# Kernel tuning notes

Measured on AMD Instinct MI355X. Metric: run time of the kernel, lower is better.

The kernel has to match this reference:

```python
import jax, jax.numpy as jnp
import numpy as np

B, S, D_H, D_L, K, K_H, W = 4, 4096, 1024, 256, 64, 4, 9


def setup_inputs() -> dict:
    key = jax.random.key(0)
    ks = jax.random.split(key, 6)
    return {
        "inputs": jax.random.normal(ks[0], (B, S, D_H), jnp.float32),
        "W1": jax.random.normal(ks[1], (D_H, D_L), jnp.float32) * 0.02,
        "b1": jnp.zeros((D_L,), jnp.float32),
        "RME": jax.random.normal(ks[2], (D_L, K), jnp.float32),
        "K2": jax.random.normal(ks[3], (K_H, D_L, D_L), jnp.float32) * 0.02,
        "b2": jnp.zeros((D_L,), jnp.float32),
        "Wu": jax.random.normal(ks[4], (D_L, D_H), jnp.float32) * 0.02,
        "bu": jnp.zeros((D_H,), jnp.float32),
        "gamma": jnp.ones((D_H,), jnp.float32),
        "beta": jnp.zeros((D_H,), jnp.float32),
    }


def _memory_reorg(act, RMVs, k_h):
    # act: [B,S,d_l], RMVs: [B,S,k]
    R = jnp.transpose(RMVs, (0, 2, 1))  # [B,k,S]
    h_vars = jnp.mean((R - jnp.mean(R, axis=-1, keepdims=True)) ** 2, axis=-1)  # [B,k]
    top = jnp.argsort(-h_vars, axis=-1)[:, :k_h]                   # [B,k_h]
    h_max = jnp.take_along_axis(R, top[:, :, None], axis=1)        # [B,k_h,S]
    perm = jnp.argsort(h_max, axis=-1)                             # [B,k_h,S] permutation indices
    g = jnp.take_along_axis(act[:, None], perm[..., None], axis=2) # [B,k_h,S,d_l]
    return jnp.transpose(g, (0, 2, 1, 3))                          # [B,S,k_h,d_l]


def reference(inputs, W1, b1, RME, K2, b2, Wu, bu, gamma, beta):
    # DOWN_PROJECTION_1
    q = jax.nn.relu(jnp.einsum('bsh,hd->bsd', inputs, W1) + b1)    # [B,S,d_l]
    # RANDOM_PROJECTION
    RMVs = jnp.einsum('bsd,dk->bsk', q, RME)                       # [B,S,k]
    # Memory reorganization (variance-based argsort permutations)
    qp = _memory_reorg(q, RMVs, K_H)                               # [B,S,k_h,d_l]
    # DOWN_PROJECTION_2
    q2 = jax.nn.relu(jnp.einsum('bskd,kde->bse', qp, K2) + b2)     # [B,S,d_l]
    # Sliding-window key construction (edge windows replicated)
    half = (W - 1) // 2
    widx = jnp.arange(S - W + 1)[:, None] + jnp.arange(W)[None, :]  # [S-W+1, W]
    win = q2[:, widx]                                               # [B,S-W+1,W,d_l]
    first = jnp.broadcast_to(q2[:, None, :W], (B, half, W, D_L))
    last = jnp.broadcast_to(q2[:, None, S - W:], (B, half, W, D_L))
    keyt = jnp.concatenate([first, win, last], axis=1)              # [B,S,W,d_l]
    # Windowed attention
    f = jnp.sqrt(jnp.float32(D_L))
    scores = jax.nn.softmax(jnp.einsum('bsd,bswd->bsw', q2, keyt) / f, axis=-1)  # [B,S,W]
    # UP_PROJECTION on keys -> values
    val = jax.nn.relu(jnp.einsum('bswd,dh->bswh', keyt, Wu) + bu)   # [B,S,W,d_h]
    out = jnp.einsum('bswh,bsw->bsh', val, scores)                  # [B,S,d_h]
    # LayerNorm (keras default epsilon=1e-3) on residual
    x = out + inputs
    mu = jnp.mean(x, axis=-1, keepdims=True)
    var = jnp.mean((x - mu) ** 2, axis=-1, keepdims=True)
    return gamma * (x - mu) * jax.lax.rsqrt(var + 1e-3) + beta
```

## Files before the change

kernel.cpp:

```cpp
#include <hip/hip_runtime.h>

#define B_  4
#define S_  4096
#define DH  1024
#define DL  256
#define KK  64
#define KH  4
#define WW  9

typedef unsigned short ushort_t;
typedef _Float16 f16;
typedef _Float16 f16x8 __attribute__((ext_vector_type(8)));
typedef float  f32x4  __attribute__((ext_vector_type(4)));

__device__ __forceinline__ void gld_lds16(const void* g, void* lds_uniform_base) {
    __builtin_amdgcn_global_load_lds(
        (const __attribute__((address_space(1))) unsigned int*)g,
        (__attribute__((address_space(3))) unsigned int*)lds_uniform_base,
        16, 0, 0);
}

template<bool AFP32, bool GATHER, int OUTMODE>
__global__ __launch_bounds__(256)
void mfma_gemm_sm(const float* __restrict__ Af,
                  const ushort_t* __restrict__ Ah, const ushort_t* __restrict__ Al,
                  const ushort_t* __restrict__ Bh, const ushort_t* __restrict__ Bl,
                  const float* __restrict__ bias, float* __restrict__ C,
                  ushort_t* __restrict__ Ch, ushort_t* __restrict__ Cl,
                  const int* __restrict__ gidx, int K, int N, int nbx)
{
    __shared__ __align__(16) ushort_t Abuf[2][64 * 64 * 2];
    __shared__ __align__(16) ushort_t Bbuf[2][2][64 * 64];

    const int tid = threadIdx.x;
    const int w = tid >> 6, l = tid & 63;
    const int wm = w >> 1, wn = w & 1;
    const int lr = l & 15, lk = l >> 4;
    const int cpx = gridDim.x >> 3;
    const int orig = (blockIdx.x & 7) * cpx + (blockIdx.x >> 3);
    const int m0 = (orig / nbx) * 64, n0 = (orig % nbx) * 64;

    int rg[2][KH];
    if (GATHER) {
        const int r0 = tid >> 3;
        #pragma unroll
        for (int it = 0; it < 2; ++it)
            #pragma unroll
            for (int h = 0; h < KH; ++h)
                rg[it][h] = gidx[(m0 + it * 32 + r0) * KH + h];
    }

    auto stage = [&](int buf, int k0) {
        if (AFP32) {
            float* Asf = (float*)Abuf[buf];
            #pragma unroll
            for (int it = 0; it < 4; ++it) {
                const int c = it * 256 + tid;
                const int r = c >> 4, cc = c & 15;
                const int cs = cc ^ ((r & 7) << 1);
                gld_lds16(Af + (size_t)(m0 + r) * K + k0 + cs * 4, &Asf[(size_t)c * 4]);
            }
        } else {
            ushort_t* Ash = Abuf[buf];
            ushort_t* Asl = Abuf[buf] + 64 * 64;
            #pragma unroll
            for (int it = 0; it < 2; ++it) {
                const int c = it * 256 + tid;
                const int r = c >> 3, kp = c & 7;
                const int kl = kp ^ (r & 7);
                size_t offA;
                if (GATHER) {
                    offA = (size_t)rg[it][k0 >> 8] * DL + (k0 & (DL - 1)) + kl * 8;
                } else {
                    offA = (size_t)(m0 + r) * K + k0 + kl * 8;
                }
                gld_lds16(Ah + offA, &Ash[(size_t)c * 8]);
                gld_lds16(Al + offA, &Asl[(size_t)c * 8]);
            }
        }
        #pragma unroll
        for (int it = 0; it < 2; ++it) {
            const int c = it * 256 + tid;
            const int r = c >> 3, kp = c & 7;
            const int kl = kp ^ (r & 7);
            const size_t off = (size_t)(n0 + r) * K + k0 + kl * 8;
            gld_lds16(Bh + off, &Bbuf[buf][0][(size_t)c * 8]);
            gld_lds16(Bl + off, &Bbuf[buf][1][(size_t)c * 8]);
        }
    };

    f32x4 acc0[2][2] = {};
    f32x4 acc1[2][2] = {};

    stage(0, 0);
    __syncthreads();
    int cur = 0;
    for (int k0 = 0; k0 < K; k0 += 64) {
        if (k0 + 64 < K) stage(cur ^ 1, k0 + 64);

        #pragma unroll
        for (int ks = 0; ks < 2; ++ks) {
            f16x8 ah[2], al[2];
            #pragma unroll
            for (int mf = 0; mf < 2; ++mf) {
                const int row = wm * 32 + mf * 16 + lr;
                const int kb  = ks * 4 + lk;
                if (AFP32) {
                    const float* Asf = (const float*)Abuf[cur];
                    const int fo = row * 64 + ((kb ^ (row & 7)) << 3);
                    const f32x4 lo = *(const f32x4*)&Asf[fo];
                    const f32x4 hi = *(const f32x4*)&Asf[fo + 4];
                    const float xs[8] = {lo[0], lo[1], lo[2], lo[3],
                                         hi[0], hi[1], hi[2], hi[3]};
                    #pragma unroll
                    for (int e = 0; e < 8; ++e) {
                        const f16 h = (f16)xs[e];
                        const f16 lv = (f16)((xs[e] - (float)h) * 2048.0f);
                        ah[mf][e] = h;
                        al[mf][e] = lv;
                    }
                } else {
                    const ushort_t* Ash = Abuf[cur];
                    const ushort_t* Asl = Abuf[cur] + 64 * 64;
                    const int o = row * 64 + ((kb ^ (row & 7)) << 3);
                    ah[mf] = *(const f16x8*)&Ash[o];
                    al[mf] = *(const f16x8*)&Asl[o];
                }
            }
            #pragma unroll
            for (int nf = 0; nf < 2; ++nf) {
                const int row = wn * 32 + nf * 16 + lr;
                const int kb  = ks * 4 + lk;
                const int o   = row * 64 + ((kb ^ (row & 7)) << 3);
                const f16x8 bh = *(const f16x8*)&Bbuf[cur][0][o];
                const f16x8 bl = *(const f16x8*)&Bbuf[cur][1][o];
                #pragma unroll
                for (int mf = 0; mf < 2; ++mf) {
                    acc0[mf][nf] = __builtin_amdgcn_mfma_f32_16x16x32_f16(
                        ah[mf], bh, acc0[mf][nf], 0, 0, 0);
                    acc1[mf][nf] = __builtin_amdgcn_mfma_f32_16x16x32_f16(
                        ah[mf], bl, acc1[mf][nf], 0, 0, 0);
                    acc1[mf][nf] = __builtin_amdgcn_mfma_f32_16x16x32_f16(
                        al[mf], bh, acc1[mf][nf], 0, 0, 0);
                }
            }
        }
        __syncthreads();
        cur ^= 1;
    }

    float bv[2];
    #pragma unroll
    for (int nf = 0; nf < 2; ++nf)
        bv[nf] = bias[n0 + wn * 32 + nf * 16 + lr];
    #pragma unroll
    for (int mf = 0; mf < 2; ++mf)
        #pragma unroll
        for (int nf = 0; nf < 2; ++nf)
            #pragma unroll
            for (int r = 0; r < 4; ++r) {
                const int m = m0 + wm * 32 + mf * 16 + lk * 4 + r;
                const int n = n0 + wn * 32 + nf * 16 + lr;
                float x = acc0[mf][nf][r] + acc1[mf][nf][r] * (1.0f / 2048.0f) + bv[nf];
                x = fmaxf(x, 0.f);
                const f16 h = (f16)x;
                if (OUTMODE == 2) {
                    Ch[(size_t)m * N + n] = __builtin_bit_cast(ushort_t, h);
                } else {
                    C[(size_t)m * N + n] = x;
                    Ch[(size_t)m * N + n] = __builtin_bit_cast(ushort_t, h);
                    const f16 lo = (f16)((x - (float)h) * 2048.0f);
                    Cl[(size_t)m * N + n] = __builtin_bit_cast(ushort_t, lo);
                }
            }
}

__global__ __launch_bounds__(512)
void mfma_gemm1l(const ushort_t* __restrict__ Ah, const ushort_t* __restrict__ Bh,
                 const float* __restrict__ bias, ushort_t* __restrict__ Ch,
                 int K, int N, int nbx)
{
    __shared__ __align__(16) ushort_t Ash[2][128 * 64];
    __shared__ __align__(16) ushort_t Bsh[2][128 * 64];

    const int tid = threadIdx.x;
    const int w = tid >> 6, l = tid & 63;
    const int wm = w >> 1, wn = w & 1;
    const int lr = l & 15, lk = l >> 4;
    const int cpx = gridDim.x >> 3;
    const int orig = (blockIdx.x & 7) * cpx + (blockIdx.x >> 3);
    const int m0 = (orig / nbx) * 128, n0 = (orig % nbx) * 128;

    auto stage = [&](int buf, int k0) {
        #pragma unroll
        for (int it = 0; it < 2; ++it) {
            const int c = it * 512 + tid;
            const int r = c >> 3, kp = c & 7;
            const int kl = kp ^ (r & 7);
            const size_t offA = (size_t)(m0 + r) * K + k0 + kl * 8;
            const size_t offB = (size_t)(n0 + r) * K + k0 + kl * 8;
            gld_lds16(Ah + offA, &Ash[buf][(size_t)c * 8]);
            gld_lds16(Bh + offB, &Bsh[buf][(size_t)c * 8]);
        }
    };

    f32x4 acc0[2][4] = {};

    stage(0, 0);
    __syncthreads();
    int cur = 0;
    for (int k0 = 0; k0 < K; k0 += 64) {
        if (k0 + 64 < K) stage(cur ^ 1, k0 + 64);

        #pragma unroll
        for (int ks = 0; ks < 2; ++ks) {
            f16x8 ah[2];
            #pragma unroll
            for (int mf = 0; mf < 2; ++mf) {
                const int row = wm * 32 + mf * 16 + lr;
                const int kb  = ks * 4 + lk;
                ah[mf] = *(const f16x8*)&Ash[cur][row * 64 + ((kb ^ (row & 7)) << 3)];
            }
            #pragma unroll
            for (int nf = 0; nf < 4; ++nf) {
                const int row = wn * 64 + nf * 16 + lr;
                const int kb  = ks * 4 + lk;
                const f16x8 bh = *(const f16x8*)&Bsh[cur][row * 64 + ((kb ^ (row & 7)) << 3)];
                #pragma unroll
                for (int mf = 0; mf < 2; ++mf)
                    acc0[mf][nf] = __builtin_amdgcn_mfma_f32_16x16x32_f16(
                        ah[mf], bh, acc0[mf][nf], 0, 0, 0);
            }
        }
        __syncthreads();
        cur ^= 1;
    }

    float bv[4];
    #pragma unroll
    for (int nf = 0; nf < 4; ++nf)
        bv[nf] = bias[n0 + wn * 64 + nf * 16 + lr];
    #pragma unroll
    for (int mf = 0; mf < 2; ++mf)
        #pragma unroll
        for (int nf = 0; nf < 4; ++nf)
            #pragma unroll
            for (int r = 0; r < 4; ++r) {
                const int m = m0 + wm * 32 + mf * 16 + lk * 4 + r;
                const int n = n0 + wn * 64 + nf * 16 + lr;
                float x = acc0[mf][nf][r] + bv[nf];
                x = fmaxf(x, 0.f);
                const f16 hcv = (f16)x;
                Ch[(size_t)m * N + n] = __builtin_bit_cast(ushort_t, hcv);
            }
}

__global__ __launch_bounds__(256)
void tsplit2_kernel(const float* __restrict__ in, ushort_t* __restrict__ t0,
                    ushort_t* __restrict__ t1, int K, int N)
{
    __shared__ float tile[32][33];
    const int t = threadIdx.x;
    const int bk = blockIdx.x * 32, bn = blockIdx.y * 32;
    const int c = t & 31, rb = t >> 5;
    #pragma unroll
    for (int i = 0; i < 4; ++i) {
        const int r = rb + i * 8;
        tile[r][c] = in[(size_t)(bk + r) * N + bn + c];
    }
    __syncthreads();
    #pragma unroll
    for (int i = 0; i < 4; ++i) {
        const int rr = rb + i * 8;
        const float x = tile[c][rr];
        const f16 hv = (f16)x;
        const f16 lv = (f16)((x - (float)hv) * 2048.0f);
        const size_t o = (size_t)(bn + rr) * K + bk + c;
        t0[o] = __builtin_bit_cast(ushort_t, hv);
        t1[o] = __builtin_bit_cast(ushort_t, lv);
    }
}

__global__ __launch_bounds__(256)
void gemm_trans_kernel(const float* __restrict__ A, const float* __restrict__ Bm,
                       float* __restrict__ C, int M, int KA, int N)
{
    constexpr int BK = 16;
    __shared__ float Asb[BK][64 + 4];
    __shared__ float Bsb[BK][64 + 4];
    const int tid = threadIdx.x;
    const int tx = tid & 15, ty = tid >> 4;
    const int m0 = blockIdx.y * 64, n0 = blockIdx.x * 64;

    float acc[4][4] = {};
    const int lr = tid >> 2, lc = (tid & 3) << 2;
    const int kr = tid >> 4, nc = (tid & 15) << 2;

    for (int k0 = 0; k0 < KA; k0 += BK) {
        const float4 a4 = *reinterpret_cast<const float4*>(A + (size_t)(m0 + lr) * KA + k0 + lc);
        const float4 b4 = *reinterpret_cast<const float4*>(Bm + (size_t)(k0 + kr) * N + n0 + nc);
        Asb[lc + 0][lr] = a4.x; Asb[lc + 1][lr] = a4.y;
        Asb[lc + 2][lr] = a4.z; Asb[lc + 3][lr] = a4.w;
        *reinterpret_cast<float4*>(&Bsb[kr][nc]) = b4;
        __syncthreads();
        #pragma unroll
        for (int kk = 0; kk < BK; ++kk) {
            const float4 av = *reinterpret_cast<const float4*>(&Asb[kk][ty << 2]);
            const float4 bv = *reinterpret_cast<const float4*>(&Bsb[kk][tx << 2]);
            const float a[4] = {av.x, av.y, av.z, av.w};
            const float b[4] = {bv.x, bv.y, bv.z, bv.w};
            #pragma unroll
            for (int i = 0; i < 4; ++i)
                #pragma unroll
                for (int j = 0; j < 4; ++j)
                    acc[i][j] = fmaf(a[i], b[j], acc[i][j]);
        }
        __syncthreads();
    }
    #pragma unroll
    for (int i = 0; i < 4; ++i) {
        const int m = m0 + (ty << 2) + i;
        const int b = m >> 12, s = m & (S_ - 1);
        #pragma unroll
        for (int j = 0; j < 4; ++j) {
            const int n = n0 + (tx << 2) + j;
            C[(size_t)(b * N + n) * S_ + s] = acc[i][j];
        }
    }
}

__global__ __launch_bounds__(256)
void var_kernel(const float* __restrict__ rmvT, float* __restrict__ hvars)
{
    const int bk = blockIdx.x;
    const float* src = rmvT + (size_t)bk * S_;
    float s1 = 0.f, s2 = 0.f;
    for (int t = threadIdx.x; t < S_; t += 256) {
        const float v = src[t];
        s1 += v; s2 += v * v;
    }
    #pragma unroll
    for (int off = 32; off; off >>= 1) {
        s1 += __shfl_xor(s1, off);
        s2 += __shfl_xor(s2, off);
    }
    __shared__ float r1[4], r2[4];
    const int wave = threadIdx.x >> 6, lane = threadIdx.x & 63;
    if (lane == 0) { r1[wave] = s1; r2[wave] = s2; }
    __syncthreads();
    if (threadIdx.x == 0) {
        const float t1 = r1[0] + r1[1] + r1[2] + r1[3];
        const float t2 = r2[0] + r2[1] + r2[2] + r2[3];
        const float mu = t1 / (float)S_;
        hvars[bk] = t2 / (float)S_ - mu * mu;
    }
}

__global__ void topk_kernel(const float* __restrict__ hvars, int* __restrict__ topidx)
{
    const int b = threadIdx.x;
    if (b >= B_) return;
    float v[KK];
    for (int k = 0; k < KK; ++k) v[k] = hvars[b * KK + k];
    for (int i = 0; i < KH; ++i) {
        int best = 0; float bv = -3.4e38f;
        for (int k = 0; k < KK; ++k)
            if (v[k] > bv) { bv = v[k]; best = k; }
        topidx[b * KH + i] = best;
        v[best] = -3.4e38f;
    }
}

__global__ __launch_bounds__(256)
void rank_kernel(const float* __restrict__ rmvT, const int* __restrict__ topidx,
                 int* __restrict__ gidx)
{
    const int bi = blockIdx.x;
    const int b = bi >> 2, ih = bi & 3;
    const int k = topidx[b * KH + ih];
    const float* src = rmvT + (size_t)(b * KK + k) * S_;
    __shared__ __align__(16) unsigned long long keys[S_];
    __shared__ int partial[4][64];
    for (int t = threadIdx.x; t < S_; t += 256) {
        const unsigned bits = __builtin_bit_cast(unsigned, src[t]);
        const unsigned u = (bits & 0x80000000u) ? ~bits : (bits | 0x80000000u);
        keys[t] = ((unsigned long long)u << 12) | (unsigned)t;
    }
    __syncthreads();

    const int il = threadIdx.x & 63;
    const int chunk = threadIdx.x >> 6;
    const int i = blockIdx.y * 64 + il;
    const unsigned long long ki = keys[i];

    int cnt = 0;
    const int jbase = chunk << 10;
    #pragma unroll 8
    for (int jj = 0; jj < 1024; jj += 2) {
        const ulonglong2 k2 = *reinterpret_cast<const ulonglong2*>(&keys[jbase + jj]);
        cnt += (int)(k2.x < ki);
        cnt += (int)(k2.y < ki);
    }
    partial[chunk][il] = cnt;
    __syncthreads();
    if (threadIdx.x < 64) {
        const int rank = partial[0][threadIdx.x] + partial[1][threadIdx.x]
                       + partial[2][threadIdx.x] + partial[3][threadIdx.x];
        const int ii = blockIdx.y * 64 + threadIdx.x;
        gidx[((b << 12) + rank) * KH + ih] = (b << 12) + ii;
    }
}

__global__ __launch_bounds__(256)
void final_kernel(const ushort_t* __restrict__ vh, const ushort_t* __restrict__ q2h,
                  const float* __restrict__ inputs, const float* __restrict__ gamma,
                  const float* __restrict__ beta, float* __restrict__ out)
{
    const int bid = blockIdx.x;
    const int m0 = (((bid & 7) << 9) | (bid >> 3)) << 2;
    const int wave = threadIdx.x >> 6, lane = threadIdx.x & 63;
    const int m = m0 + wave;
    const int s = m & (S_ - 1), b = m >> 12;
    const int jb = (s < 4) ? 0 : (s >= S_ - 4 ? S_ - WW : s - 4);

    const ushort_t* vb = vh + (size_t)(b * S_ + jb) * DH;
    const float* inp = inputs + (size_t)m * DH;
    f16x8 varr[2][WW];
    float4 iv[2][2];
    #pragma unroll
    for (int c = 0; c < 2; ++c) {
        const int h = (c << 9) + (lane << 3);
        #pragma unroll
        for (int w = 0; w < WW; ++w)
            varr[c][w] = *reinterpret_cast<const f16x8*>(vb + (size_t)w * DH + h);
        iv[c][0] = *reinterpret_cast<const float4*>(inp + h);
        iv[c][1] = *reinterpret_cast<const float4*>(inp + h + 4);
    }

    const ushort4 qv4 = *reinterpret_cast<const ushort4*>(q2h + (size_t)m * DL + (lane << 2));
    const float qx = (float)__builtin_bit_cast(f16, qv4.x);
    const float qy = (float)__builtin_bit_cast(f16, qv4.y);
    const float qz = (float)__builtin_bit_cast(f16, qv4.z);
    const float qw = (float)__builtin_bit_cast(f16, qv4.w);
    const ushort_t* kbase = q2h + (size_t)(b * S_ + jb) * DL;
    float sc[WW];
    #pragma unroll
    for (int w = 0; w < WW; ++w) {
        const ushort4 kv4 = *reinterpret_cast<const ushort4*>(kbase + w * DL + (lane << 2));
        float d = qx * (float)__builtin_bit_cast(f16, kv4.x)
                + qy * (float)__builtin_bit_cast(f16, kv4.y)
                + qz * (float)__builtin_bit_cast(f16, kv4.z)
                + qw * (float)__builtin_bit_cast(f16, kv4.w);
        #pragma unroll
        for (int off = 32; off; off >>= 1) d += __shfl_xor(d, off);
        sc[w] = d * 0.0625f;
    }
    float mx = sc[0];
    #pragma unroll
    for (int w = 1; w < WW; ++w) mx = fmaxf(mx, sc[w]);
    float wgt[WW]; float sum = 0.f;
    #pragma unroll
    for (int w = 0; w < WW; ++w) { wgt[w] = __expf(sc[w] - mx); sum += wgt[w]; }
    const float inv = 1.f / sum;
    #pragma unroll
    for (int w = 0; w < WW; ++w) wgt[w] *= inv;

    float x[2][8];
    float s1 = 0.f, s2 = 0.f;
    #pragma unroll
    for (int c = 0; c < 2; ++c) {
        float acc[8] = {};
        #pragma unroll
        for (int w = 0; w < WW; ++w) {
            const f16x8 vv = varr[c][w];
            #pragma unroll
            for (int e = 0; e < 8; ++e)
                acc[e] = fmaf(wgt[w], (float)vv[e], acc[e]);
        }
        #pragma unroll
        for (int e = 0; e < 8; ++e) {
            const float ivv = (e < 4) ? (&iv[c][0].x)[e] : (&iv[c][1].x)[e - 4];
            acc[e] += ivv;
            x[c][e] = acc[e];
            s1 += acc[e];
            s2 += acc[e] * acc[e];
        }
    }

    #pragma unroll
    for (int off = 32; off; off >>= 1) {
        s1 += __shfl_xor(s1, off);
        s2 += __shfl_xor(s2, off);
    }
    const float mu = s1 / (float)DH;
    const float rs = rsqrtf(s2 / (float)DH - mu * mu + 0.001f);

    #pragma unroll
    for (int c = 0; c < 2; ++c) {
        const int h = (c << 9) + (lane << 3);
        #pragma unroll
        for (int half = 0; half < 2; ++half) {
            const float4 g  = *reinterpret_cast<const float4*>(gamma + h + half * 4);
            const float4 bt = *reinterpret_cast<const float4*>(beta + h + half * 4);
            float4 o;
            o.x = g.x * (x[c][half * 4 + 0] - mu) * rs + bt.x;
            o.y = g.y * (x[c][half * 4 + 1] - mu) * rs + bt.y;
            o.z = g.z * (x[c][half * 4 + 2] - mu) * rs + bt.z;
            o.w = g.w * (x[c][half * 4 + 3] - mu) * rs + bt.w;
            *reinterpret_cast<float4*>(out + (size_t)m * DH + h + half * 4) = o;
        }
    }
}

extern "C" void kernel_launch(void* const* d_in, const int* in_sizes, int n_in,
                              void* d_out, int out_size, void* d_ws, size_t ws_size,
                              hipStream_t stream)
{
    (void)in_sizes; (void)n_in; (void)out_size; (void)ws_size;
    const float* inputs = (const float*)d_in[0];
    const float* W1     = (const float*)d_in[1];
    const float* b1     = (const float*)d_in[2];
    const float* RME    = (const float*)d_in[3];
    const float* K2     = (const float*)d_in[4];
    const float* b2     = (const float*)d_in[5];
    const float* Wu     = (const float*)d_in[6];
    const float* bu     = (const float*)d_in[7];
    const float* gamma  = (const float*)d_in[8];
    const float* beta   = (const float*)d_in[9];
    float* out = (float*)d_out;

    char* ws = (char*)d_ws;
    const size_t MB = 1u << 20;
    ushort_t* vh  = (ushort_t*)(ws + 0 * MB);
    float*    q   = (float*)   (ws + 64 * MB);
    ushort_t* qh  = (ushort_t*)(ws + 80 * MB);
    ushort_t* ql  = (ushort_t*)(ws + 88 * MB);
    ushort_t* q2h = (ushort_t*)(ws + 112 * MB);
    float*    rmvT= (float*)   (ws + 128 * MB);
    float*    hvars  = (float*)(ws + 132 * MB);
    int*      topidx = (int*)  (ws + 132 * MB + 4096);
    int*      gidx   = (int*)  (ws + 132 * MB + 8192);
    ushort_t* w1th = (ushort_t*)(ws + 133 * MB);
    ushort_t* w1tl = w1th + (DH * DL);
    ushort_t* k2th = w1tl + (DH * DL);
    ushort_t* k2tl = k2th + (KH * DL * DL);
    ushort_t* wuth = k2tl + (KH * DL * DL);
    ushort_t* wutl = wuth + (DL * DH);

    const int M = B_ * S_;

    tsplit2_kernel<<<dim3(DH / 32, DL / 32), dim3(256), 0, stream>>>(W1, w1th, w1tl, DH, DL);
    tsplit2_kernel<<<dim3(KH * DL / 32, DL / 32), dim3(256), 0, stream>>>((const float*)K2, k2th, k2tl, KH * DL, DL);
    tsplit2_kernel<<<dim3(DL / 32, DH / 32), dim3(256), 0, stream>>>(Wu, wuth, wutl, DL, DH);

    mfma_gemm_sm<true, false, 1><<<dim3((DL / 64) * (M / 64)), dim3(256), 0, stream>>>(
        inputs, nullptr, nullptr, w1th, w1tl, b1, q, qh, ql, nullptr, DH, DL, DL / 64);
    gemm_trans_kernel<<<dim3(KK / 64, M / 64), dim3(256), 0, stream>>>(q, RME, rmvT, M, DL, KK);
    var_kernel<<<dim3(B_ * KK), dim3(256), 0, stream>>>(rmvT, hvars);
    topk_kernel<<<dim3(1), dim3(64), 0, stream>>>(hvars, topidx);
    rank_kernel<<<dim3(B_ * KH, S_ / 64), dim3(256), 0, stream>>>(rmvT, topidx, gidx);
    mfma_gemm_sm<false, true, 2><<<dim3((DL / 64) * (M / 64)), dim3(256), 0, stream>>>(
        nullptr, qh, ql, k2th, k2tl, b2, nullptr, q2h, nullptr, gidx, KH * DL, DL, DL / 64);
    mfma_gemm1l<<<dim3((DH / 128) * (M / 128)), dim3(512), 0, stream>>>(
        q2h, wuth, bu, vh, DL, DH, DH / 128);
    final_kernel<<<dim3(M / 4), dim3(256), 0, stream>>>(vh, q2h, inputs, gamma, beta, out);
}
```

Baseline: 195.6 us.

## Load A operands directly into registers and drop double-buffering in up-projection GEMM

```diff
diff --git a/kernel.cpp b/kernel.cpp
--- a/kernel.cpp
+++ b/kernel.cpp
@@ -20,16 +20,16 @@
         16, 0, 0);
 }
 
-template<bool AFP32, bool GATHER, int OUTMODE>
+template<bool AFP32, bool GATHER, int OUTMODE, int KT>
 __global__ __launch_bounds__(256)
-void mfma_gemm_sm(const float* __restrict__ Af,
+void gemm_adirect(const float* __restrict__ Af,
                   const ushort_t* __restrict__ Ah, const ushort_t* __restrict__ Al,
                   const ushort_t* __restrict__ Bh, const ushort_t* __restrict__ Bl,
                   const float* __restrict__ bias, float* __restrict__ C,
                   ushort_t* __restrict__ Ch, ushort_t* __restrict__ Cl,
-                  const int* __restrict__ gidx, int K, int N, int nbx)
-{
-    __shared__ __align__(16) ushort_t Abuf[2][64 * 64 * 2];
+                  const int* __restrict__ gidx, int N, int nbx)
+{
+    constexpr int NT = KT / 64;
     __shared__ __align__(16) ushort_t Bbuf[2][2][64 * 64];
 
     const int tid = threadIdx.x;
@@ -39,92 +39,66 @@
     const int cpx = gridDim.x >> 3;
     const int orig = (blockIdx.x & 7) * cpx + (blockIdx.x >> 3);
     const int m0 = (orig / nbx) * 64, n0 = (orig % nbx) * 64;
-
-    int rg[2][KH];
-    if (GATHER) {
-        const int r0 = tid >> 3;
-        #pragma unroll
-        for (int it = 0; it < 2; ++it)
-            #pragma unroll
-            for (int h = 0; h < KH; ++h)
-                rg[it][h] = gidx[(m0 + it * 32 + r0) * KH + h];
-    }
-
-    auto stage = [&](int buf, int k0) {
-        if (AFP32) {
-            float* Asf = (float*)Abuf[buf];
-            #pragma unroll
-            for (int it = 0; it < 4; ++it) {
-                const int c = it * 256 + tid;
-                const int r = c >> 4, cc = c & 15;
-                const int cs = cc ^ ((r & 7) << 1);
-                gld_lds16(Af + (size_t)(m0 + r) * K + k0 + cs * 4, &Asf[(size_t)c * 4]);
-            }
-        } else {
-            ushort_t* Ash = Abuf[buf];
-            ushort_t* Asl = Abuf[buf] + 64 * 64;
-            #pragma unroll
-            for (int it = 0; it < 2; ++it) {
-                const int c = it * 256 + tid;
-                const int r = c >> 3, kp = c & 7;
-                const int kl = kp ^ (r & 7);
-                size_t offA;
-                if (GATHER) {
-                    offA = (size_t)rg[it][k0 >> 8] * DL + (k0 & (DL - 1)) + kl * 8;
-                } else {
-                    offA = (size_t)(m0 + r) * K + k0 + kl * 8;
-                }
-                gld_lds16(Ah + offA, &Ash[(size_t)c * 8]);
-                gld_lds16(Al + offA, &Asl[(size_t)c * 8]);
-            }
-        }
+    const int ar0 = m0 + wm * 32 + lr;
+
+    f32x4 af0[2][2][2], af1[2][2][2];
+    f16x8 ahr0[2][2], alr0[2][2], ahr1[2][2], alr1[2][2];
+
+    auto stageB = [&](int buf, int k0) {
         #pragma unroll
         for (int it = 0; it < 2; ++it) {
             const int c = it * 256 + tid;
             const int r = c >> 3, kp = c & 7;
             const int kl = kp ^ (r & 7);
-            const size_t off = (size_t)(n0 + r) * K + k0 + kl * 8;
+            const size_t off = (size_t)(n0 + r) * KT + k0 + kl * 8;
             gld_lds16(Bh + off, &Bbuf[buf][0][(size_t)c * 8]);
             gld_lds16(Bl + off, &Bbuf[buf][1][(size_t)c * 8]);
         }
     };
+    auto loadAf = [&](f32x4 ar[2][2][2], int k0) {
+        #pragma unroll
+        for (int mf = 0; mf < 2; ++mf)
+            #pragma unroll
+            for (int ks = 0; ks < 2; ++ks) {
+                const float* p = Af + (size_t)(ar0 + mf * 16) * KT + k0 + ks * 32 + lk * 8;
+                ar[mf][ks][0] = *(const f32x4*)p;
+                ar[mf][ks][1] = *(const f32x4*)(p + 4);
+            }
+    };
+    auto loadAg = [&](f16x8 ha[2][2], f16x8 la[2][2], int k0) {
+        const int head = k0 >> 8, kk = k0 & (DL - 1);
+        #pragma unroll
+        for (int mf = 0; mf < 2; ++mf) {
+            const int row = gidx[(ar0 + mf * 16) * KH + head];
+            #pragma unroll
+            for (int ks = 0; ks < 2; ++ks) {
+                const size_t off = (size_t)row * DL + kk + ks * 32 + lk * 8;
+                ha[mf][ks] = *(const f16x8*)(Ah + off);
+                la[mf][ks] = *(const f16x8*)(Al + off);
+            }
+        }
+    };
 
     f32x4 acc0[2][2] = {};
     f32x4 acc1[2][2] = {};
 
-    stage(0, 0);
-    __syncthreads();
-    int cur = 0;
-    for (int k0 = 0; k0 < K; k0 += 64) {
-        if (k0 + 64 < K) stage(cur ^ 1, k0 + 64);
-
+    auto computeT = [&](f32x4 arf[2][2][2], f16x8 arh[2][2], f16x8 arl[2][2], int buf) {
         #pragma unroll
         for (int ks = 0; ks < 2; ++ks) {
             f16x8 ah[2], al[2];
             #pragma unroll
             for (int mf = 0; mf < 2; ++mf) {
-                const int row = wm * 32 + mf * 16 + lr;
-                const int kb  = ks * 4 + lk;
                 if (AFP32) {
-                    const float* Asf = (const float*)Abuf[cur];
-                    const int fo = row * 64 + ((kb ^ (row & 7)) << 3);
-                    const f32x4 lo = *(const f32x4*)&Asf[fo];
-                    const f32x4 hi = *(const f32x4*)&Asf[fo + 4];
-                    const float xs[8] = {lo[0], lo[1], lo[2], lo[3],
-                                         hi[0], hi[1], hi[2], hi[3]};
                     #pragma unroll
                     for (int e = 0; e < 8; ++e) {
-                        const f16 h = (f16)xs[e];
-                        const f16 lv = (f16)((xs[e] - (float)h) * 2048.0f);
+                        const float xv = (e < 4) ? arf[mf][ks][0][e] : arf[mf][ks][1][e - 4];
+                        const f16 h = (f16)xv;
                         ah[mf][e] = h;
-                        al[mf][e] = lv;
+                        al[mf][e] = (f16)((xv - (float)h) * 2048.0f);
                     }
                 } else {
-                    const ushort_t* Ash = Abuf[cur];
-                    const ushort_t* Asl = Abuf[cur] + 64 * 64;
-                    const int o = row * 64 + ((kb ^ (row & 7)) << 3);
-                    ah[mf] = *(const f16x8*)&Ash[o];
-                    al[mf] = *(const f16x8*)&Asl[o];
+                    ah[mf] = arh[mf][ks];
+                    al[mf] = arl[mf][ks];
                 }
             }
             #pragma unroll
@@ -132,8 +106,8 @@
                 const int row = wn * 32 + nf * 16 + lr;
                 const int kb  = ks * 4 + lk;
                 const int o   = row * 64 + ((kb ^ (row & 7)) << 3);
-                const f16x8 bh = *(const f16x8*)&Bbuf[cur][0][o];
-                const f16x8 bl = *(const f16x8*)&Bbuf[cur][1][o];
+                const f16x8 bh = *(const f16x8*)&Bbuf[buf][0][o];
+                const f16x8 bl = *(const f16x8*)&Bbuf[buf][1][o];
                 #pragma unroll
                 for (int mf = 0; mf < 2; ++mf) {
                     acc0[mf][nf] = __builtin_amdgcn_mfma_f32_16x16x32_f16(
@@ -145,8 +119,36 @@
                 }
             }
         }
-        __syncthreads();
-        cur ^= 1;
+    };
+
+    stageB(0, 0);
+    if (AFP32) loadAf(af0, 0); else loadAg(ahr0, alr0, 0);
+    asm volatile("s_waitcnt vmcnt(0)" ::: "memory");
+    __builtin_amdgcn_s_barrier();
+    __builtin_amdgcn_sched_barrier(0);
+
+    #pragma unroll 1
+    for (int t = 0; t < NT; t += 2) {
+        if (t + 1 < NT) {
+            stageB(1, (t + 1) * 64);
+            if (AFP32) loadAf(af1, (t + 1) * 64); else loadAg(ahr1, alr1, (t + 1) * 64);
+        }
+        computeT(af0, ahr0, alr0, 0);
+        if (t + 1 < NT) { asm volatile("s_waitcnt vmcnt(8)" ::: "memory"); }
+        else            { asm volatile("s_waitcnt vmcnt(0)" ::: "memory"); }
+        __builtin_amdgcn_s_barrier();
+        __builtin_amdgcn_sched_barrier(0);
+        if (t + 1 < NT) {
+            if (t + 2 < NT) {
+                stageB(0, (t + 2) * 64);
+                if (AFP32) loadAf(af0, (t + 2) * 64); else loadAg(ahr0, alr0, (t + 2) * 64);
+            }
+            computeT(af1, ahr1, alr1, 1);
+            if (t + 2 < NT) { asm volatile("s_waitcnt vmcnt(8)" ::: "memory"); }
+            else            { asm volatile("s_waitcnt vmcnt(0)" ::: "memory"); }
+            __builtin_amdgcn_s_barrier();
+            __builtin_amdgcn_sched_barrier(0);
+        }
     }
 
     float bv[2];
@@ -180,8 +182,8 @@
                  const float* __restrict__ bias, ushort_t* __restrict__ Ch,
                  int K, int N, int nbx)
 {
-    __shared__ __align__(16) ushort_t Ash[2][128 * 64];
-    __shared__ __align__(16) ushort_t Bsh[2][128 * 64];
+    __shared__ __align__(16) ushort_t Ash[128 * 64];
+    __shared__ __align__(16) ushort_t Bsh[128 * 64];
 
     const int tid = threadIdx.x;
     const int w = tid >> 6, l = tid & 63;
@@ -191,7 +193,9 @@
     const int orig = (blockIdx.x & 7) * cpx + (blockIdx.x >> 3);
     const int m0 = (orig / nbx) * 128, n0 = (orig % nbx) * 128;
 
-    auto stage = [&](int buf, int k0) {
+    f32x4 acc0[2][4] = {};
+
+    for (int k0 = 0; k0 < K; k0 += 64) {
         #pragma unroll
         for (int it = 0; it < 2; ++it) {
             const int c = it * 512 + tid;
@@ -199,18 +203,10 @@
             const int kl = kp ^ (r & 7);
             const size_t offA = (size_t)(m0 + r) * K + k0 + kl * 8;
             const size_t offB = (size_t)(n0 + r) * K + k0 + kl * 8;
-            gld_lds16(Ah + offA, &Ash[buf][(size_t)c * 8]);
-            gld_lds16(Bh + offB, &Bsh[buf][(size_t)c * 8]);
-        }
-    };
-
-    f32x4 acc0[2][4] = {};
-
-    stage(0, 0);
-    __syncthreads();
-    int cur = 0;
-    for (int k0 = 0; k0 < K; k0 += 64) {
-        if (k0 + 64 < K) stage(cur ^ 1, k0 + 64);
+            gld_lds16(Ah + offA, &Ash[(size_t)c * 8]);
+            gld_lds16(Bh + offB, &Bsh[(size_t)c * 8]);
+        }
+        __syncthreads();
 
         #pragma unroll
         for (int ks = 0; ks < 2; ++ks) {
@@ -219,13 +215,13 @@
             for (int mf = 0; mf < 2; ++mf) {
                 const int row = wm * 32 + mf * 16 + lr;
                 const int kb  = ks * 4 + lk;
-                ah[mf] = *(const f16x8*)&Ash[cur][row * 64 + ((kb ^ (row & 7)) << 3)];
+                ah[mf] = *(const f16x8*)&Ash[row * 64 + ((kb ^ (row & 7)) << 3)];
             }
             #pragma unroll
             for (int nf = 0; nf < 4; ++nf) {
                 const int row = wn * 64 + nf * 16 + lr;
                 const int kb  = ks * 4 + lk;
-                const f16x8 bh = *(const f16x8*)&Bsh[cur][row * 64 + ((kb ^ (row & 7)) << 3)];
+                const f16x8 bh = *(const f16x8*)&Bsh[row * 64 + ((kb ^ (row & 7)) << 3)];
                 #pragma unroll
                 for (int mf = 0; mf < 2; ++mf)
                     acc0[mf][nf] = __builtin_amdgcn_mfma_f32_16x16x32_f16(
@@ -233,7 +229,6 @@
             }
         }
         __syncthreads();
-        cur ^= 1;
     }
 
     float bv[4];
@@ -553,14 +548,14 @@
     tsplit2_kernel<<<dim3(KH * DL / 32, DL / 32), dim3(256), 0, stream>>>((const float*)K2, k2th, k2tl, KH * DL, DL);
     tsplit2_kernel<<<dim3(DL / 32, DH / 32), dim3(256), 0, stream>>>(Wu, wuth, wutl, DL, DH);
 
-    mfma_gemm_sm<true, false, 1><<<dim3((DL / 64) * (M / 64)), dim3(256), 0, stream>>>(
-        inputs, nullptr, nullptr, w1th, w1tl, b1, q, qh, ql, nullptr, DH, DL, DL / 64);
+    gemm_adirect<true, false, 1, DH><<<dim3((DL / 64) * (M / 64)), dim3(256), 0, stream>>>(
+        inputs, nullptr, nullptr, w1th, w1tl, b1, q, qh, ql, nullptr, DL, DL / 64);
     gemm_trans_kernel<<<dim3(KK / 64, M / 64), dim3(256), 0, stream>>>(q, RME, rmvT, M, DL, KK);
     var_kernel<<<dim3(B_ * KK), dim3(256), 0, stream>>>(rmvT, hvars);
     topk_kernel<<<dim3(1), dim3(64), 0, stream>>>(hvars, topidx);
     rank_kernel<<<dim3(B_ * KH, S_ / 64), dim3(256), 0, stream>>>(rmvT, topidx, gidx);
-    mfma_gemm_sm<false, true, 2><<<dim3((DL / 64) * (M / 64)), dim3(256), 0, stream>>>(
-        nullptr, qh, ql, k2th, k2tl, b2, nullptr, q2h, nullptr, gidx, KH * DL, DL, DL / 64);
+    gemm_adirect<false, true, 2, KH * DL><<<dim3((DL / 64) * (M / 64)), dim3(256), 0, stream>>>(
+        nullptr, qh, ql, k2th, k2tl, b2, nullptr, q2h, nullptr, gidx, DL, DL / 64);
     mfma_gemm1l<<<dim3((DH / 128) * (M / 128)), dim3(512), 0, stream>>>(
         q2h, wuth, bu, vh, DL, DH, DH / 128);
     final_kernel<<<dim3(M / 4), dim3(256), 0, stream>>>(vh, q2h, inputs, gamma, beta, out);
```

New measurement: 265.4 us. 35.7% more time.
